# Kernel tuning notes

Measured on AMD Instinct MI355X. Metric: run time of the kernel, lower is better.

Reference implementation:

```python
import jax, jax.numpy as jnp
import numpy as np

N = 50000      # num nodes
E = 800000     # num edges (before self loops)
B = 50         # num graphs in batch
F_IN = 15
C = 64         # hidden_channels
H = 4          # num_heads
NEG_SLOPE = 0.2  # PyG GATConv default


def setup_inputs() -> dict:
    key = jax.random.key(0)
    ks = jax.random.split(key, 32)
    s = 0.05
    inp = {
        "x": jax.random.normal(ks[0], (N, F_IN), dtype=jnp.float32),
        "edge_index": jax.random.randint(ks[1], (2, E), 0, N, dtype=jnp.int32),
        "batch": jnp.sort(jax.random.randint(ks[2], (N,), 0, B, dtype=jnp.int32)),
        "W1": jax.random.normal(ks[3], (F_IN, H * C)) * s,
        "aS1": jax.random.normal(ks[4], (H, C)) * s,
        "aD1": jax.random.normal(ks[5], (H, C)) * s,
        "b1": jnp.zeros((H * C,)),
        "W2": jax.random.normal(ks[6], (H * C, H * C)) * s,
        "aS2": jax.random.normal(ks[7], (H, C)) * s,
        "aD2": jax.random.normal(ks[8], (H, C)) * s,
        "b2": jnp.zeros((H * C,)),
        # GAT layer 3: 256 -> 64, 1 head
        "W3": jax.random.normal(ks[9], (H * C, C)) * s,
        "aS3": jax.random.normal(ks[10], (1, C)) * s,
        "aD3": jax.random.normal(ks[11], (1, C)) * s,
        "b3": jnp.zeros((C,)),
        # node attention MLP: 64 -> 32 -> 1
        "Wna1": jax.random.normal(ks[12], (C, 32)) * s,
        "bna1": jnp.zeros((32,)),
        "Wna2": jax.random.normal(ks[13], (32, 1)) * s,
        "bna2": jnp.zeros((1,)),
        # graph classifier: 128 -> 128 -> 64 -> 1
        "Wc1": jax.random.normal(ks[14], (2 * C, 128)) * s,
        "bc1": jnp.zeros((128,)),
        "Wc2": jax.random.normal(ks[15], (128, 64)) * s,
        "bc2": jnp.zeros((64,)),
        "Wc3": jax.random.normal(ks[16], (64, 1)) * s,
        "bc3": jnp.zeros((1,)),
    }
    return inp


def _gat_conv(x, src, dst, W, a_src, a_dst, b, heads, ch):
    """PyG-style GATConv (add_self_loops=True, negative_slope=0.2, eval mode)."""
    n = x.shape[0]
    h = (x @ W).reshape(n, heads, ch)               # [N, H, C]
    alpha_s = jnp.einsum('nhc,hc->nh', h, a_src)    # per-node src score
    alpha_d = jnp.einsum('nhc,hc->nh', h, a_dst)
    loops = jnp.arange(n, dtype=src.dtype)
    s = jnp.concatenate([src, loops])               # [E+N]
    d = jnp.concatenate([dst, loops])
    e = jax.nn.leaky_relu(alpha_s[s] + alpha_d[d], NEG_SLOPE)   # [E+N, H]
    # segment softmax over incoming edges of each dst node
    m = jax.ops.segment_max(e, d, num_segments=n)
    ex = jnp.exp(e - m[d])
    denom = jax.ops.segment_sum(ex, d, num_segments=n)
    alpha = ex / denom[d]                           # [E+N, H]
    msg = h[s] * alpha[:, :, None]                  # [E+N, H, C]
    out = jax.ops.segment_sum(msg, d, num_segments=n)  # [N, H, C]
    return out.reshape(n, heads * ch) + b


def reference(x, edge_index, batch, W1, aS1, aD1, b1, W2, aS2, aD2, b2,
              W3, aS3, aD3, b3, Wna1, bna1, Wna2, bna2,
              Wc1, bc1, Wc2, bc2, Wc3, bc3):
    src, dst = edge_index[0], edge_index[1]
    x1 = jax.nn.elu(_gat_conv(x, src, dst, W1, aS1, aD1, b1, H, C))
    x2 = jax.nn.elu(_gat_conv(x1, src, dst, W2, aS2, aD2, b2, H, C))
    x3 = jax.nn.elu(_gat_conv(x2, src, dst, W3, aS3, aD3, b3, 1, C))  # [N, 64]

    # node attention: MLP then softmax over ALL nodes (dim=0, as in source)
    na = jax.nn.relu(x3 @ Wna1 + bna1) @ Wna2 + bna2   # [N, 1]
    node_attention = jax.nn.softmax(na, axis=0)

    # graph pooling
    ones = jnp.ones((x3.shape[0],), dtype=x3.dtype)
    cnt = jax.ops.segment_sum(ones, batch, num_segments=B)         # [B]
    mean = jax.ops.segment_sum(x3, batch, num_segments=B) / jnp.maximum(cnt, 1.0)[:, None]
    mx = jax.ops.segment_max(x3, batch, num_segments=B)
    mx = jnp.where(cnt[:, None] > 0, mx, 0.0)
    g = jnp.concatenate([mean, mx], axis=1)                        # [B, 128]

    h1 = jax.nn.relu(g @ Wc1 + bc1)
    h2 = jax.nn.relu(h1 @ Wc2 + bc2)
    risk = jax.nn.sigmoid(h2 @ Wc3 + bc3)                          # [B, 1]
    return (risk, node_attention)
```

## Files before the change

### kernel.cpp

```cpp
#include <hip/hip_runtime.h>
#include <math.h>

#define NN 50000
#define NP 50176
#define EE 800000
#define ETOT (EE + NN)
#define BB 50
#define PC 16
#define NGRP 12500

typedef unsigned short u16;
typedef unsigned char u8;
typedef __attribute__((ext_vector_type(8))) short short8;
typedef __attribute__((ext_vector_type(4))) float floatx4;
typedef __attribute__((ext_vector_type(2))) float floatx2;

__device__ __forceinline__ float b2f(u16 u) {
  return __int_as_float(((int)u) << 16);
}
__device__ __forceinline__ u16 f2b(float f) {
  unsigned u = __float_as_uint(f);
  unsigned r = (u + 0x7fffu + ((u >> 16) & 1u)) >> 16;
  return (u16)r;
}
__device__ __forceinline__ u8 f2f8(float v) {
  return (u8)(__builtin_amdgcn_cvt_pk_fp8_f32(v, v, 0, false) & 0xFF);
}
__device__ __forceinline__ float readlane_f(float v, int l) {
  return __int_as_float(__builtin_amdgcn_readlane(__float_as_int(v), l));
}

__global__ void count_kernel(const int* __restrict__ ei, int* __restrict__ cnt) {
  int e = blockIdx.x * blockDim.x + threadIdx.x;
  if (e >= ETOT) return;
  int d = (e < EE) ? ei[EE + e] : (e - EE);
  atomicAdd(&cnt[d], 1);
}

__global__ void scan1_kernel(const int* __restrict__ cnt, int* __restrict__ rowp,
                             int* __restrict__ part) {
  __shared__ int s[512];
  int t = threadIdx.x;
  int i = blockIdx.x * 512 + t;
  int v = (i < NN) ? cnt[i] : 0;
  s[t] = v;
  __syncthreads();
  for (int off = 1; off < 512; off <<= 1) {
    int add = (t >= off) ? s[t - off] : 0;
    __syncthreads();
    s[t] += add;
    __syncthreads();
  }
  if (i < NN) rowp[i] = s[t] - v;
  if (t == 511) part[blockIdx.x] = s[511];
}

__global__ void scan2_kernel(int* __restrict__ part, int* __restrict__ rowp) {
  __shared__ int s[128];
  int t = threadIdx.x;
  int v = (t < 98) ? part[t] : 0;
  s[t] = v;
  __syncthreads();
  for (int off = 1; off < 128; off <<= 1) {
    int add = (t >= off) ? s[t - off] : 0;
    __syncthreads();
    s[t] += add;
    __syncthreads();
  }
  if (t < 98) part[t] = s[t] - v;
  if (t == 97) rowp[NN] = s[97];
}

__global__ void scan3_kernel(int* __restrict__ rowp, const int* __restrict__ part) {
  int i = blockIdx.x * 512 + threadIdx.x;
  if (i < NN) rowp[i] += part[blockIdx.x];
}

__global__ void fill_kernel(const int* __restrict__ ei, const int* __restrict__ rowp,
                            int* __restrict__ cur, int* __restrict__ col) {
  int e = blockIdx.x * blockDim.x + threadIdx.x;
  if (e >= ETOT) return;
  int s, d;
  if (e < EE) { s = ei[e]; d = ei[EE + e]; } else { s = e - EE; d = s; }
  int p = atomicAdd(&cur[d], 1);
  col[rowp[d] + p] = s;
}

__global__ void prep_kernel(const float* __restrict__ x, const float* __restrict__ W1,
                            const float* __restrict__ W2, const float* __restrict__ W3,
                            u16* __restrict__ xb, u16* __restrict__ W1t,
                            u16* __restrict__ W2t, u16* __restrict__ W3t) {
  const int T0 = NP * 32, T1 = T0 + 8192, T2 = T1 + 65536, T3 = T2 + 16384;
  int i = blockIdx.x * 256 + threadIdx.x;
  if (i < T0) {
    int n = i >> 5, c = i & 31;
    xb[i] = (n < NN && c < 15) ? f2b(x[n * 15 + c]) : (u16)0;
  } else if (i < T1) {
    int j = i - T0, n = j >> 5, k = j & 31;
    W1t[j] = (k < 15) ? f2b(W1[k * 256 + n]) : (u16)0;
  } else if (i < T2) {
    int j = i - T1, n = j >> 8, k = j & 255;
    W2t[j] = f2b(W2[k * 256 + n]);
  } else if (i < T3) {
    int j = i - T2, n = j >> 8, k = j & 255;
    W3t[j] = f2b(W3[k * 64 + n]);
  }
}

template <int BK, bool F8>
__global__ __launch_bounds__(256) void gemm_bf16_kernel(
    const u16* __restrict__ A, const u16* __restrict__ Bt, u16* __restrict__ C,
    u8* __restrict__ C8, int K, int N, const float* __restrict__ aS,
    const float* __restrict__ aD, float* __restrict__ as_o,
    float* __restrict__ ad_o, int Hh) {
  __shared__ u16 Al[128][BK + 8];
  __shared__ u16 Bl[64][BK + 8];
  __shared__ float sS[4][64], sD[4][64];
  int R0 = blockIdx.x * 128, C0 = blockIdx.y * 64;
  int wid = threadIdx.x >> 6, lane = threadIdx.x & 63;
  int wr = (wid >> 1) * 64, wc = (wid & 1) * 32;
  int lrow = lane & 15, lk8 = (lane >> 4) * 8;
  int rq = (lane >> 4) * 4;
  const int Q4 = BK / 4;
  const int nA = 128 * Q4, nB = 64 * Q4;
  floatx4 acc[4][2];
#pragma unroll
  for (int i = 0; i < 4; ++i)
#pragma unroll
    for (int j = 0; j < 2; ++j) acc[i][j] = (floatx4){0.f, 0.f, 0.f, 0.f};

  for (int k0 = 0; k0 < K; k0 += BK) {
    for (int c = threadIdx.x; c < nA + nB; c += 256) {
      if (c < nA) {
        int r = c / Q4, o = (c % Q4) * 4;
        *(ushort4*)&Al[r][o] = *(const ushort4*)&A[(size_t)(R0 + r) * K + k0 + o];
      } else {
        int c2 = c - nA;
        int r = c2 / Q4, o = (c2 % Q4) * 4;
        *(ushort4*)&Bl[r][o] = *(const ushort4*)&Bt[(size_t)(C0 + r) * K + k0 + o];
      }
    }
    __syncthreads();
#pragma unroll
    for (int ks = 0; ks < BK / 32; ++ks) {
      short8 a[4], b[2];
#pragma unroll
      for (int i = 0; i < 4; ++i) a[i] = *(const short8*)&Al[wr + i * 16 + lrow][ks * 32 + lk8];
#pragma unroll
      for (int j = 0; j < 2; ++j) b[j] = *(const short8*)&Bl[wc + j * 16 + lrow][ks * 32 + lk8];
#pragma unroll
      for (int i = 0; i < 4; ++i)
#pragma unroll
        for (int j = 0; j < 2; ++j)
          acc[i][j] = __builtin_amdgcn_mfma_f32_16x16x32_bf16(a[i], b[j], acc[i][j], 0, 0, 0);
    }
    __syncthreads();
  }
#pragma unroll
  for (int i = 0; i < 4; ++i)
#pragma unroll
    for (int j = 0; j < 2; ++j)
#pragma unroll
      for (int q = 0; q < 4; ++q) {
        int gr = R0 + wr + i * 16 + rq + q;
        int gc = C0 + wc + j * 16 + lrow;
        if constexpr (F8)
          C8[(size_t)gr * N + gc] = f2f8(acc[i][j][q]);
        else
          C[(size_t)gr * N + gc] = f2b(acc[i][j][q]);
      }
  int hb = blockIdx.y * 64;
  float wS0 = aS[hb + wc + lrow], wS1 = aS[hb + wc + 16 + lrow];
  float wD0 = aD[hb + wc + lrow], wD1 = aD[hb + wc + 16 + lrow];
#pragma unroll
  for (int i = 0; i < 4; ++i)
#pragma unroll
    for (int q = 0; q < 4; ++q) {
      float vS = acc[i][0][q] * wS0 + acc[i][1][q] * wS1;
      float vD = acc[i][0][q] * wD0 + acc[i][1][q] * wD1;
#pragma unroll
      for (int o = 8; o; o >>= 1) {
        vS += __shfl_xor(vS, o, 64);
        vD += __shfl_xor(vD, o, 64);
      }
      if (lrow == 0) {
        int rl = i * 16 + rq + q;
        sS[wid][rl] = vS;
        sD[wid][rl] = vD;
      }
    }
  __syncthreads();
  if (threadIdx.x < 128) {
    int p = threadIdx.x >> 6, r = threadIdx.x & 63;
    int gr = R0 + p * 64 + r;
    as_o[(size_t)gr * Hh + blockIdx.y] = sS[2 * p][r] + sS[2 * p + 1][r];
    ad_o[(size_t)gr * Hh + blockIdx.y] = sD[2 * p][r] + sD[2 * p + 1][r];
  }
}

__global__ __launch_bounds__(256) void agg4_kernel(
    const u8* __restrict__ h8, const float* __restrict__ as_i,
    const float* __restrict__ ad_i, const int* __restrict__ rowp,
    const int* __restrict__ col, const float* __restrict__ bias,
    u16* __restrict__ xo) {
  __shared__ float exs[4][64][4];
  int wid = threadIdx.x >> 6, lane = threadIdx.x & 63;
  int hj = lane >> 4;
  int lq = lane << 2;
  for (int g = blockIdx.x; g < NGRP; g += gridDim.x) {
    int d = g * 4 + wid;
    int rp0 = rowp[d], deg = rowp[d + 1] - rp0;
    float4 add = *(const float4*)&ad_i[(size_t)d * 4];
    float a0 = 0.f, a1 = 0.f, a2 = 0.f, a3 = 0.f;
    float den0 = 0.f, den1 = 0.f, den2 = 0.f, den3 = 0.f;

    for (int base = 0; base < deg; base += 64) {
      int i = base + lane;
      bool valid = i < deg;
      int s = valid ? col[rp0 + i] : 0;
      float4 asv = *(const float4*)&as_i[(size_t)s * 4];
      float e0 = asv.x + add.x, e1 = asv.y + add.y, e2 = asv.z + add.z, e3 = asv.w + add.w;
      e0 = (e0 > 0.f) ? e0 : 0.2f * e0;
      e1 = (e1 > 0.f) ? e1 : 0.2f * e1;
      e2 = (e2 > 0.f) ? e2 : 0.2f * e2;
      e3 = (e3 > 0.f) ? e3 : 0.2f * e3;
      float x0 = valid ? __expf(e0) : 0.f;
      float x1 = valid ? __expf(e1) : 0.f;
      float x2 = valid ? __expf(e2) : 0.f;
      float x3 = valid ? __expf(e3) : 0.f;
      den0 += x0; den1 += x1; den2 += x2; den3 += x3;
      *(float4*)&exs[wid][lane][0] = make_float4(x0, x1, x2, x3);
      __threadfence_block();
      int cnt = min(64, deg - base);
      int k8 = cnt & ~7;
      for (int k = 0; k < k8; k += 8) {
        unsigned wv[8];
        float qv[8];
#pragma unroll
        for (int u = 0; u < 8; ++u) {
          int sk = __builtin_amdgcn_readlane(s, k + u);
          qv[u] = exs[wid][k + u][hj];
          wv[u] = *(const unsigned*)&h8[(size_t)sk * 256 + lq];
        }
#pragma unroll
        for (int u = 0; u < 8; ++u) {
          floatx2 lo = __builtin_amdgcn_cvt_pk_f32_fp8(wv[u], false);
          floatx2 hi = __builtin_amdgcn_cvt_pk_f32_fp8(wv[u], true);
          a0 += qv[u] * lo.x;
          a1 += qv[u] * lo.y;
          a2 += qv[u] * hi.x;
          a3 += qv[u] * hi.y;
        }
      }
      for (int k = k8; k < cnt; ++k) {
        int sk = __builtin_amdgcn_readlane(s, k);
        float qk = exs[wid][k][hj];
        unsigned wv = *(const unsigned*)&h8[(size_t)sk * 256 + lq];
        floatx2 lo = __builtin_amdgcn_cvt_pk_f32_fp8(wv, false);
        floatx2 hi = __builtin_amdgcn_cvt_pk_f32_fp8(wv, true);
        a0 += qk * lo.x;
        a1 += qk * lo.y;
        a2 += qk * hi.x;
        a3 += qk * hi.y;
      }
    }
#pragma unroll
    for (int o = 32; o; o >>= 1) {
      den0 += __shfl_xor(den0, o, 64);
      den1 += __shfl_xor(den1, o, 64);
      den2 += __shfl_xor(den2, o, 64);
      den3 += __shfl_xor(den3, o, 64);
    }
    float den = (hj == 0) ? den0 : (hj == 1) ? den1 : (hj == 2) ? den2 : den3;
    float inv = 1.f / den;
    float4 bv = *(const float4*)&bias[lq];
    float v0 = a0 * inv + bv.x;
    float v1 = a1 * inv + bv.y;
    float v2 = a2 * inv + bv.z;
    float v3 = a3 * inv + bv.w;
    v0 = (v0 > 0.f) ? v0 : expm1f(v0);
    v1 = (v1 > 0.f) ? v1 : expm1f(v1);
    v2 = (v2 > 0.f) ? v2 : expm1f(v2);
    v3 = (v3 > 0.f) ? v3 : expm1f(v3);
    ushort4 o4;
    o4.x = f2b(v0); o4.y = f2b(v1); o4.z = f2b(v2); o4.w = f2b(v3);
    ((ushort4*)xo)[(size_t)d * 64 + lane] = o4;
  }
}

__global__ __launch_bounds__(256) void agg1na_kernel(
    const u16* __restrict__ h, const float* __restrict__ as_i,
    const float* __restrict__ ad_i, const int* __restrict__ rowp,
    const int* __restrict__ col, const float* __restrict__ bias,
    float* __restrict__ xo, const float* __restrict__ Wna1,
    const float* __restrict__ bna1, const float* __restrict__ Wna2,
    const float* __restrict__ bna2, float* __restrict__ na) {
  __shared__ float Ws[2048];
  __shared__ float W2s[32];
  __shared__ float xrow[4][64];
  for (int i = threadIdx.x; i < 2048; i += 256) Ws[i] = Wna1[i];
  if (threadIdx.x < 32) W2s[threadIdx.x] = Wna2[threadIdx.x];
  __syncthreads();
  int wid = threadIdx.x >> 6, lane = threadIdx.x & 63;
  float b1v = bna1[lane & 31];
  float b2v = bna2[0];
  for (int g = blockIdx.x; g < NGRP; g += gridDim.x) {
    int d = g * 4 + wid;
    int rp0 = rowp[d], deg = rowp[d + 1] - rp0;
    float add = ad_i[d];
    float acc = 0.f, den = 0.f;
    for (int base = 0; base < deg; base += 64) {
      int i = base + lane;
      bool valid = i < deg;
      int s = valid ? col[rp0 + i] : 0;
      float e = as_i[s] + add;
      e = (e > 0.f) ? e : 0.2f * e;
      float ex = valid ? __expf(e) : 0.f;
      den += ex;
      int cnt = min(64, deg - base);
      int k8 = cnt & ~7;
      for (int k = 0; k < k8; k += 8) {
        int sA[8];
        float qA[8], hv[8];
#pragma unroll
        for (int u = 0; u < 8; ++u) {
          sA[u] = __builtin_amdgcn_readlane(s, k + u);
          qA[u] = readlane_f(ex, k + u);
        }
#pragma unroll
        for (int u = 0; u < 8; ++u) hv[u] = b2f(h[(size_t)sA[u] * 64 + lane]);
        float p0 = qA[0] * hv[0] + qA[1] * hv[1];
        float p1 = qA[2] * hv[2] + qA[3] * hv[3];
        float p2 = qA[4] * hv[4] + qA[5] * hv[5];
        float p3 = qA[6] * hv[6] + qA[7] * hv[7];
        acc += (p0 + p1) + (p2 + p3);
      }
      for (int k = k8; k < cnt; ++k) {
        int sk = __builtin_amdgcn_readlane(s, k);
        float qk = readlane_f(ex, k);
        acc += qk * b2f(h[(size_t)sk * 64 + lane]);
      }
    }
#pragma unroll
    for (int o = 32; o; o >>= 1) den += __shfl_xor(den, o, 64);
    float v = acc / den + bias[lane];
    v = (v > 0.f) ? v : expm1f(v);
    xo[(size_t)d * 64 + lane] = v;
    xrow[wid][lane] = v;
    __threadfence_block();
    int j = lane & 31;
    int coff = (lane >> 5) * 32;
    float hj = 0.f;
#pragma unroll
    for (int c = 0; c < 32; ++c) hj += xrow[wid][coff + c] * Ws[(coff + c) * 32 + j];
    hj += __shfl_xor(hj, 32, 64);
    hj += b1v;
    float r = fmaxf(hj, 0.f) * W2s[j];
#pragma unroll
    for (int o = 16; o; o >>= 1) r += __shfl_xor(r, o, 64);
    if (lane == 0) na[d] = __expf(r + b2v);
  }
}

__global__ void na_sum_kernel(const float* __restrict__ na, float* __restrict__ gsum) {
  __shared__ float s[4];
  float acc = 0.f;
  for (int i = blockIdx.x * blockDim.x + threadIdx.x; i < NN; i += gridDim.x * blockDim.x)
    acc += na[i];
  for (int o = 32; o; o >>= 1) acc += __shfl_xor(acc, o, 64);
  int wid = threadIdx.x >> 6, lane = threadIdx.x & 63;
  if (lane == 0) s[wid] = acc;
  __syncthreads();
  if (threadIdx.x == 0) atomicAdd(gsum, s[0] + s[1] + s[2] + s[3]);
}

__global__ void na_write_kernel(const float* __restrict__ na, const float* __restrict__ gsum,
                                float* __restrict__ out) {
  int n = blockIdx.x * blockDim.x + threadIdx.x;
  if (n >= NN) return;
  out[n] = na[n] / gsum[0];
}

__global__ void pool1_kernel(const float* __restrict__ x3, const int* __restrict__ batch,
                             float* __restrict__ ppsum, float* __restrict__ ppmax) {
  int b = blockIdx.x, c = blockIdx.y;
  int lane = threadIdx.x & 63, wid = threadIdx.x >> 6;
  int lo = 0, hi = NN;
  while (lo < hi) { int m = (lo + hi) >> 1; if (batch[m] < b) lo = m + 1; else hi = m; }
  int start = lo;
  lo = start; hi = NN;
  while (lo < hi) { int m = (lo + hi) >> 1; if (batch[m] < b + 1) lo = m + 1; else hi = m; }
  int end = lo;
  int len = end - start;
  int c0 = start + (int)((long)len * c / PC);
  int c1 = start + (int)((long)len * (c + 1) / PC);
  float acc = 0.f, mx = -INFINITY;
  for (int n = c0 + wid; n < c1; n += 4) {
    float v = x3[(size_t)n * 64 + lane];
    acc += v;
    mx = fmaxf(mx, v);
  }
  __shared__ float ssum[4][64], smax[4][64];
  ssum[wid][lane] = acc;
  smax[wid][lane] = mx;
  __syncthreads();
  if (wid == 0) {
    acc = ssum[0][lane] + ssum[1][lane] + ssum[2][lane] + ssum[3][lane];
    mx = fmaxf(fmaxf(smax[0][lane], smax[1][lane]), fmaxf(smax[2][lane], smax[3][lane]));
    size_t o = ((size_t)c * BB + b) * 64 + lane;
    ppsum[o] = acc;
    ppmax[o] = mx;
  }
}

__global__ void pool2cls_kernel(const float* __restrict__ ppsum, const float* __restrict__ ppmax,
                                const int* __restrict__ batch, const float* __restrict__ Wc1,
                                const float* __restrict__ bc1, const float* __restrict__ Wc2,
                                const float* __restrict__ bc2, const float* __restrict__ Wc3,
                                const float* __restrict__ bc3, float* __restrict__ out) {
  __shared__ float g[128], h1[128], h2[64], scnt;
  int b = blockIdx.x, t = threadIdx.x;
  if (t == 0) {
    int lo = 0, hi = NN;
    while (lo < hi) { int m = (lo + hi) >> 1; if (batch[m] < b) lo = m + 1; else hi = m; }
    int start = lo;
    lo = start; hi = NN;
    while (lo < hi) { int m = (lo + hi) >> 1; if (batch[m] < b + 1) lo = m + 1; else hi = m; }
    scnt = (float)(lo - start);
  }
  float s = 0.f, m = -INFINITY;
  if (t < 64) {
#pragma unroll
    for (int c = 0; c < PC; ++c) {
      size_t o = ((size_t)c * BB + b) * 64 + t;
      s += ppsum[o];
      m = fmaxf(m, ppmax[o]);
    }
  }
  __syncthreads();
  float cnt = scnt;
  if (t < 64) {
    g[t] = (cnt > 0.f) ? s / fmaxf(cnt, 1.f) : 0.f;
    g[64 + t] = (cnt > 0.f) ? m : 0.f;
  }
  __syncthreads();
  float v = bc1[t];
  for (int k = 0; k < 128; ++k) v += g[k] * Wc1[k * 128 + t];
  h1[t] = fmaxf(v, 0.f);
  __syncthreads();
  if (t < 64) {
    float v2 = bc2[t];
    for (int k = 0; k < 128; ++k) v2 += h1[k] * Wc2[k * 64 + t];
    h2[t] = fmaxf(v2, 0.f);
  }
  __syncthreads();
  if (t == 0) {
    float z = bc3[0];
    for (int k = 0; k < 64; ++k) z += h2[k] * Wc3[k];
    out[b] = 1.f / (1.f + expf(-z));
  }
}

extern "C" void kernel_launch(void* const* d_in, const int* in_sizes, int n_in,
                              void* d_out, int out_size, void* d_ws, size_t ws_size,
                              hipStream_t stream) {
  const float* x    = (const float*)d_in[0];
  const int*   ei   = (const int*)d_in[1];
  const int*   batch= (const int*)d_in[2];
  const float* W1 = (const float*)d_in[3];
  const float* aS1= (const float*)d_in[4];
  const float* aD1= (const float*)d_in[5];
  const float* b1 = (const float*)d_in[6];
  const float* W2 = (const float*)d_in[7];
  const float* aS2= (const float*)d_in[8];
  const float* aD2= (const float*)d_in[9];
  const float* b2 = (const float*)d_in[10];
  const float* W3 = (const float*)d_in[11];
  const float* aS3= (const float*)d_in[12];
  const float* aD3= (const float*)d_in[13];
  const float* b3 = (const float*)d_in[14];
  const float* Wna1=(const float*)d_in[15];
  const float* bna1=(const float*)d_in[16];
  const float* Wna2=(const float*)d_in[17];
  const float* bna2=(const float*)d_in[18];
  const float* Wc1=(const float*)d_in[19];
  const float* bc1=(const float*)d_in[20];
  const float* Wc2=(const float*)d_in[21];
  const float* bc2=(const float*)d_in[22];
  const float* Wc3=(const float*)d_in[23];
  const float* bc3=(const float*)d_in[24];
  float* out = (float*)d_out;

  char* w = (char*)d_ws;
  size_t off = 0;
  auto alloc = [&](size_t bytes) {
    void* p = w + off;
    off = (off + bytes + 255) & ~(size_t)255;
    return p;
  };
  u16* xb   = (u16*)alloc((size_t)NP * 32 * 2);
  u16* bufA = (u16*)alloc((size_t)NP * 256 * 2);
  u16* bufB = (u16*)alloc((size_t)NP * 256 * 2);
  u8*  h8   = (u8*)alloc((size_t)NP * 256);
  u16* W1t  = (u16*)alloc((size_t)256 * 32 * 2);
  u16* W2t  = (u16*)alloc((size_t)256 * 256 * 2);
  u16* W3t  = (u16*)alloc((size_t)64 * 256 * 2);
  float* asb  = (float*)alloc((size_t)NP * 4 * 4);
  float* adb  = (float*)alloc((size_t)NP * 4 * 4);
  float* nab  = (float*)alloc((size_t)NN * 4);
  int* rowp = (int*)alloc((size_t)(NN + 1) * 4);
  int* cntb = (int*)alloc((size_t)NN * 4);
  int* curb = (int*)alloc((size_t)NN * 4);
  float* gsum = (float*)alloc(256);
  size_t zspan = (size_t)((char*)gsum + 256 - (char*)cntb);
  int* colb = (int*)alloc((size_t)ETOT * 4);
  int* part = (int*)alloc(128 * 4);
  float* ppsum = (float*)alloc((size_t)PC * BB * 64 * 4);
  float* ppmax = (float*)alloc((size_t)PC * BB * 64 * 4);
  float* x3 = (float*)bufB;
  (void)ws_size; (void)in_sizes; (void)n_in; (void)out_size;

  hipMemsetAsync(cntb, 0, zspan, stream);

  count_kernel<<<(ETOT + 255) / 256, 256, 0, stream>>>(ei, cntb);
  scan1_kernel<<<98, 512, 0, stream>>>(cntb, rowp, part);
  scan2_kernel<<<1, 128, 0, stream>>>(part, rowp);
  scan3_kernel<<<98, 512, 0, stream>>>(rowp, part);
  fill_kernel<<<(ETOT + 255) / 256, 256, 0, stream>>>(ei, rowp, curb, colb);

  const int PREP_TOT = NP * 32 + 8192 + 65536 + 16384;
  prep_kernel<<<(PREP_TOT + 255) / 256, 256, 0, stream>>>(x, W1, W2, W3, xb, W1t, W2t, W3t);

  const int GX = NP / 128;
  const int PG = 2048;
  gemm_bf16_kernel<32, true><<<dim3(GX, 4), 256, 0, stream>>>(
      xb, W1t, nullptr, h8, 32, 256, aS1, aD1, asb, adb, 4);
  agg4_kernel<<<PG, 256, 0, stream>>>(h8, asb, adb, rowp, colb, b1, bufB);
  gemm_bf16_kernel<64, true><<<dim3(GX, 4), 256, 0, stream>>>(
      bufB, W2t, nullptr, h8, 256, 256, aS2, aD2, asb, adb, 4);
  agg4_kernel<<<PG, 256, 0, stream>>>(h8, asb, adb, rowp, colb, b2, bufB);
  gemm_bf16_kernel<64, false><<<dim3(GX, 1), 256, 0, stream>>>(
      bufB, W3t, bufA, nullptr, 256, 64, aS3, aD3, asb, adb, 1);
  agg1na_kernel<<<PG, 256, 0, stream>>>(bufA, asb, adb, rowp, colb, b3, x3,
                                        Wna1, bna1, Wna2, bna2, nab);

  na_sum_kernel<<<196, 256, 0, stream>>>(nab, gsum);
  na_write_kernel<<<(NN + 255) / 256, 256, 0, stream>>>(nab, gsum, out + BB);
  pool1_kernel<<<dim3(BB, PC), 256, 0, stream>>>(x3, batch, ppsum, ppmax);
  pool2cls_kernel<<<BB, 128, 0, stream>>>(ppsum, ppmax, batch, Wc1, bc1, Wc2, bc2,
                                          Wc3, bc3, out);
}
```

Baseline: 389.0 us.

## Precompute edge attention exponentials in separate per-edge kernels before aggregation

```diff
diff --git a/kernel.cpp b/kernel.cpp
--- a/kernel.cpp
+++ b/kernel.cpp
@@ -7,7 +7,6 @@
 #define ETOT (EE + NN)
 #define BB 50
 #define PC 16
-#define NGRP 12500
 
 typedef unsigned short u16;
 typedef unsigned char u8;
@@ -77,13 +76,16 @@
 }
 
 __global__ void fill_kernel(const int* __restrict__ ei, const int* __restrict__ rowp,
-                            int* __restrict__ cur, int* __restrict__ col) {
+                            int* __restrict__ cur, int* __restrict__ col,
+                            int* __restrict__ dstb) {
   int e = blockIdx.x * blockDim.x + threadIdx.x;
   if (e >= ETOT) return;
   int s, d;
   if (e < EE) { s = ei[e]; d = ei[EE + e]; } else { s = e - EE; d = s; }
   int p = atomicAdd(&cur[d], 1);
-  col[rowp[d] + p] = s;
+  int idx = rowp[d] + p;
+  col[idx] = s;
+  dstb[idx] = d;
 }
 
 __global__ void prep_kernel(const float* __restrict__ x, const float* __restrict__ W1,
@@ -198,103 +200,118 @@
   }
 }
 
+template <int LAYER>
+__global__ void escore4_kernel(const float* __restrict__ as_i, const float* __restrict__ ad_i,
+                               const int* __restrict__ col, const int* __restrict__ dstb,
+                               float4* __restrict__ exl) {
+  int i = blockIdx.x * 256 + threadIdx.x;
+  if (i >= ETOT) return;
+  int s = col[i], d = dstb[i];
+  float4 a = *(const float4*)&as_i[(size_t)s * 4];
+  float4 b = *(const float4*)&ad_i[(size_t)d * 4];
+  float e0 = a.x + b.x, e1 = a.y + b.y, e2 = a.z + b.z, e3 = a.w + b.w;
+  e0 = (e0 > 0.f) ? e0 : 0.2f * e0;
+  e1 = (e1 > 0.f) ? e1 : 0.2f * e1;
+  e2 = (e2 > 0.f) ? e2 : 0.2f * e2;
+  e3 = (e3 > 0.f) ? e3 : 0.2f * e3;
+  exl[i] = make_float4(__expf(e0), __expf(e1), __expf(e2), __expf(e3));
+}
+
+__global__ void escore1_kernel(const float* __restrict__ as_i, const float* __restrict__ ad_i,
+                               const int* __restrict__ col, const int* __restrict__ dstb,
+                               float* __restrict__ exl) {
+  int i = blockIdx.x * 256 + threadIdx.x;
+  if (i >= ETOT) return;
+  float e = as_i[col[i]] + ad_i[dstb[i]];
+  e = (e > 0.f) ? e : 0.2f * e;
+  exl[i] = __expf(e);
+}
+
+template <int LAYER>
 __global__ __launch_bounds__(256) void agg4_kernel(
-    const u8* __restrict__ h8, const float* __restrict__ as_i,
-    const float* __restrict__ ad_i, const int* __restrict__ rowp,
-    const int* __restrict__ col, const float* __restrict__ bias,
-    u16* __restrict__ xo) {
+    const u8* __restrict__ h8, const float4* __restrict__ exl,
+    const int* __restrict__ rowp, const int* __restrict__ col,
+    const float* __restrict__ bias, u16* __restrict__ xo) {
   __shared__ float exs[4][64][4];
   int wid = threadIdx.x >> 6, lane = threadIdx.x & 63;
+  int d = blockIdx.x * 4 + wid;
+  int rp0 = rowp[d], deg = rowp[d + 1] - rp0;
   int hj = lane >> 4;
   int lq = lane << 2;
-  for (int g = blockIdx.x; g < NGRP; g += gridDim.x) {
-    int d = g * 4 + wid;
-    int rp0 = rowp[d], deg = rowp[d + 1] - rp0;
-    float4 add = *(const float4*)&ad_i[(size_t)d * 4];
-    float a0 = 0.f, a1 = 0.f, a2 = 0.f, a3 = 0.f;
-    float den0 = 0.f, den1 = 0.f, den2 = 0.f, den3 = 0.f;
-
-    for (int base = 0; base < deg; base += 64) {
-      int i = base + lane;
-      bool valid = i < deg;
-      int s = valid ? col[rp0 + i] : 0;
-      float4 asv = *(const float4*)&as_i[(size_t)s * 4];
-      float e0 = asv.x + add.x, e1 = asv.y + add.y, e2 = asv.z + add.z, e3 = asv.w + add.w;
-      e0 = (e0 > 0.f) ? e0 : 0.2f * e0;
-      e1 = (e1 > 0.f) ? e1 : 0.2f * e1;
-      e2 = (e2 > 0.f) ? e2 : 0.2f * e2;
-      e3 = (e3 > 0.f) ? e3 : 0.2f * e3;
-      float x0 = valid ? __expf(e0) : 0.f;
-      float x1 = valid ? __expf(e1) : 0.f;
-      float x2 = valid ? __expf(e2) : 0.f;
-      float x3 = valid ? __expf(e3) : 0.f;
-      den0 += x0; den1 += x1; den2 += x2; den3 += x3;
-      *(float4*)&exs[wid][lane][0] = make_float4(x0, x1, x2, x3);
-      __threadfence_block();
-      int cnt = min(64, deg - base);
-      int k8 = cnt & ~7;
-      for (int k = 0; k < k8; k += 8) {
-        unsigned wv[8];
-        float qv[8];
-#pragma unroll
-        for (int u = 0; u < 8; ++u) {
-          int sk = __builtin_amdgcn_readlane(s, k + u);
-          qv[u] = exs[wid][k + u][hj];
-          wv[u] = *(const unsigned*)&h8[(size_t)sk * 256 + lq];
-        }
-#pragma unroll
-        for (int u = 0; u < 8; ++u) {
-          floatx2 lo = __builtin_amdgcn_cvt_pk_f32_fp8(wv[u], false);
-          floatx2 hi = __builtin_amdgcn_cvt_pk_f32_fp8(wv[u], true);
-          a0 += qv[u] * lo.x;
-          a1 += qv[u] * lo.y;
-          a2 += qv[u] * hi.x;
-          a3 += qv[u] * hi.y;
-        }
-      }
-      for (int k = k8; k < cnt; ++k) {
-        int sk = __builtin_amdgcn_readlane(s, k);
-        float qk = exs[wid][k][hj];
-        unsigned wv = *(const unsigned*)&h8[(size_t)sk * 256 + lq];
-        floatx2 lo = __builtin_amdgcn_cvt_pk_f32_fp8(wv, false);
-        floatx2 hi = __builtin_amdgcn_cvt_pk_f32_fp8(wv, true);
-        a0 += qk * lo.x;
-        a1 += qk * lo.y;
-        a2 += qk * hi.x;
-        a3 += qk * hi.y;
-      }
-    }
-#pragma unroll
-    for (int o = 32; o; o >>= 1) {
-      den0 += __shfl_xor(den0, o, 64);
-      den1 += __shfl_xor(den1, o, 64);
-      den2 += __shfl_xor(den2, o, 64);
-      den3 += __shfl_xor(den3, o, 64);
-    }
-    float den = (hj == 0) ? den0 : (hj == 1) ? den1 : (hj == 2) ? den2 : den3;
-    float inv = 1.f / den;
-    float4 bv = *(const float4*)&bias[lq];
-    float v0 = a0 * inv + bv.x;
-    float v1 = a1 * inv + bv.y;
-    float v2 = a2 * inv + bv.z;
-    float v3 = a3 * inv + bv.w;
-    v0 = (v0 > 0.f) ? v0 : expm1f(v0);
-    v1 = (v1 > 0.f) ? v1 : expm1f(v1);
-    v2 = (v2 > 0.f) ? v2 : expm1f(v2);
-    v3 = (v3 > 0.f) ? v3 : expm1f(v3);
-    ushort4 o4;
-    o4.x = f2b(v0); o4.y = f2b(v1); o4.z = f2b(v2); o4.w = f2b(v3);
-    ((ushort4*)xo)[(size_t)d * 64 + lane] = o4;
-  }
+  float a0 = 0.f, a1 = 0.f, a2 = 0.f, a3 = 0.f;
+  float den0 = 0.f, den1 = 0.f, den2 = 0.f, den3 = 0.f;
+
+  for (int base = 0; base < deg; base += 64) {
+    int i = base + lane;
+    bool valid = i < deg;
+    int s = valid ? col[rp0 + i] : 0;
+    float4 xv = valid ? exl[rp0 + i] : make_float4(0.f, 0.f, 0.f, 0.f);
+    den0 += xv.x; den1 += xv.y; den2 += xv.z; den3 += xv.w;
+    *(float4*)&exs[wid][lane][0] = xv;
+    __threadfence_block();
+    int cnt = min(64, deg - base);
+    int k8 = cnt & ~7;
+    for (int k = 0; k < k8; k += 8) {
+      unsigned wv[8];
+      float qv[8];
+#pragma unroll
+      for (int u = 0; u < 8; ++u) {
+        int sk = __builtin_amdgcn_readlane(s, k + u);
+        qv[u] = exs[wid][k + u][hj];
+        wv[u] = *(const unsigned*)&h8[(size_t)sk * 256 + lq];
+      }
+#pragma unroll
+      for (int u = 0; u < 8; ++u) {
+        floatx2 lo = __builtin_amdgcn_cvt_pk_f32_fp8(wv[u], false);
+        floatx2 hi = __builtin_amdgcn_cvt_pk_f32_fp8(wv[u], true);
+        a0 += qv[u] * lo.x;
+        a1 += qv[u] * lo.y;
+        a2 += qv[u] * hi.x;
+        a3 += qv[u] * hi.y;
+      }
+    }
+    for (int k = k8; k < cnt; ++k) {
+      int sk = __builtin_amdgcn_readlane(s, k);
+      float qk = exs[wid][k][hj];
+      unsigned wv = *(const unsigned*)&h8[(size_t)sk * 256 + lq];
+      floatx2 lo = __builtin_amdgcn_cvt_pk_f32_fp8(wv, false);
+      floatx2 hi = __builtin_amdgcn_cvt_pk_f32_fp8(wv, true);
+      a0 += qk * lo.x;
+      a1 += qk * lo.y;
+      a2 += qk * hi.x;
+      a3 += qk * hi.y;
+    }
+  }
+#pragma unroll
+  for (int o = 32; o; o >>= 1) {
+    den0 += __shfl_xor(den0, o, 64);
+    den1 += __shfl_xor(den1, o, 64);
+    den2 += __shfl_xor(den2, o, 64);
+    den3 += __shfl_xor(den3, o, 64);
+  }
+  float den = (hj == 0) ? den0 : (hj == 1) ? den1 : (hj == 2) ? den2 : den3;
+  float inv = 1.f / den;
+  float4 bv = *(const float4*)&bias[lq];
+  float v0 = a0 * inv + bv.x;
+  float v1 = a1 * inv + bv.y;
+  float v2 = a2 * inv + bv.z;
+  float v3 = a3 * inv + bv.w;
+  v0 = (v0 > 0.f) ? v0 : expm1f(v0);
+  v1 = (v1 > 0.f) ? v1 : expm1f(v1);
+  v2 = (v2 > 0.f) ? v2 : expm1f(v2);
+  v3 = (v3 > 0.f) ? v3 : expm1f(v3);
+  ushort4 o4;
+  o4.x = f2b(v0); o4.y = f2b(v1); o4.z = f2b(v2); o4.w = f2b(v3);
+  ((ushort4*)xo)[(size_t)d * 64 + lane] = o4;
 }
 
 __global__ __launch_bounds__(256) void agg1na_kernel(
-    const u16* __restrict__ h, const float* __restrict__ as_i,
-    const float* __restrict__ ad_i, const int* __restrict__ rowp,
-    const int* __restrict__ col, const float* __restrict__ bias,
-    float* __restrict__ xo, const float* __restrict__ Wna1,
-    const float* __restrict__ bna1, const float* __restrict__ Wna2,
-    const float* __restrict__ bna2, float* __restrict__ na) {
+    const u16* __restrict__ h, const float* __restrict__ exl,
+    const int* __restrict__ rowp, const int* __restrict__ col,
+    const float* __restrict__ bias, float* __restrict__ xo,
+    const float* __restrict__ Wna1, const float* __restrict__ bna1,
+    const float* __restrict__ Wna2, const float* __restrict__ bna2,
+    float* __restrict__ na) {
   __shared__ float Ws[2048];
   __shared__ float W2s[32];
   __shared__ float xrow[4][64];
@@ -302,64 +319,57 @@
   if (threadIdx.x < 32) W2s[threadIdx.x] = Wna2[threadIdx.x];
   __syncthreads();
   int wid = threadIdx.x >> 6, lane = threadIdx.x & 63;
-  float b1v = bna1[lane & 31];
-  float b2v = bna2[0];
-  for (int g = blockIdx.x; g < NGRP; g += gridDim.x) {
-    int d = g * 4 + wid;
-    int rp0 = rowp[d], deg = rowp[d + 1] - rp0;
-    float add = ad_i[d];
-    float acc = 0.f, den = 0.f;
-    for (int base = 0; base < deg; base += 64) {
-      int i = base + lane;
-      bool valid = i < deg;
-      int s = valid ? col[rp0 + i] : 0;
-      float e = as_i[s] + add;
-      e = (e > 0.f) ? e : 0.2f * e;
-      float ex = valid ? __expf(e) : 0.f;
-      den += ex;
-      int cnt = min(64, deg - base);
-      int k8 = cnt & ~7;
-      for (int k = 0; k < k8; k += 8) {
-        int sA[8];
-        float qA[8], hv[8];
-#pragma unroll
-        for (int u = 0; u < 8; ++u) {
-          sA[u] = __builtin_amdgcn_readlane(s, k + u);
-          qA[u] = readlane_f(ex, k + u);
-        }
-#pragma unroll
-        for (int u = 0; u < 8; ++u) hv[u] = b2f(h[(size_t)sA[u] * 64 + lane]);
-        float p0 = qA[0] * hv[0] + qA[1] * hv[1];
-        float p1 = qA[2] * hv[2] + qA[3] * hv[3];
-        float p2 = qA[4] * hv[4] + qA[5] * hv[5];
-        float p3 = qA[6] * hv[6] + qA[7] * hv[7];
-        acc += (p0 + p1) + (p2 + p3);
-      }
-      for (int k = k8; k < cnt; ++k) {
-        int sk = __builtin_amdgcn_readlane(s, k);
-        float qk = readlane_f(ex, k);
-        acc += qk * b2f(h[(size_t)sk * 64 + lane]);
-      }
-    }
-#pragma unroll
-    for (int o = 32; o; o >>= 1) den += __shfl_xor(den, o, 64);
-    float v = acc / den + bias[lane];
-    v = (v > 0.f) ? v : expm1f(v);
-    xo[(size_t)d * 64 + lane] = v;
-    xrow[wid][lane] = v;
-    __threadfence_block();
-    int j = lane & 31;
-    int coff = (lane >> 5) * 32;
-    float hj = 0.f;
-#pragma unroll
-    for (int c = 0; c < 32; ++c) hj += xrow[wid][coff + c] * Ws[(coff + c) * 32 + j];
-    hj += __shfl_xor(hj, 32, 64);
-    hj += b1v;
-    float r = fmaxf(hj, 0.f) * W2s[j];
-#pragma unroll
-    for (int o = 16; o; o >>= 1) r += __shfl_xor(r, o, 64);
-    if (lane == 0) na[d] = __expf(r + b2v);
-  }
+  int d = blockIdx.x * 4 + wid;
+  int rp0 = rowp[d], deg = rowp[d + 1] - rp0;
+  float acc = 0.f, den = 0.f;
+  for (int base = 0; base < deg; base += 64) {
+    int i = base + lane;
+    bool valid = i < deg;
+    int s = valid ? col[rp0 + i] : 0;
+    float ex = valid ? exl[rp0 + i] : 0.f;
+    den += ex;
+    int cnt = min(64, deg - base);
+    int k8 = cnt & ~7;
+    for (int k = 0; k < k8; k += 8) {
+      int sA[8];
+      float qA[8], hv[8];
+#pragma unroll
+      for (int u = 0; u < 8; ++u) {
+        sA[u] = __builtin_amdgcn_readlane(s, k + u);
+        qA[u] = readlane_f(ex, k + u);
+      }
+#pragma unroll
+      for (int u = 0; u < 8; ++u) hv[u] = b2f(h[(size_t)sA[u] * 64 + lane]);
+      float p0 = qA[0] * hv[0] + qA[1] * hv[1];
+      float p1 = qA[2] * hv[2] + qA[3] * hv[3];
+      float p2 = qA[4] * hv[4] + qA[5] * hv[5];
+      float p3 = qA[6] * hv[6] + qA[7] * hv[7];
+      acc += (p0 + p1) + (p2 + p3);
+    }
+    for (int k = k8; k < cnt; ++k) {
+      int sk = __builtin_amdgcn_readlane(s, k);
+      float qk = readlane_f(ex, k);
+      acc += qk * b2f(h[(size_t)sk * 64 + lane]);
+    }
+  }
+#pragma unroll
+  for (int o = 32; o; o >>= 1) den += __shfl_xor(den, o, 64);
+  float v = acc / den + bias[lane];
+  v = (v > 0.f) ? v : expm1f(v);
+  xo[(size_t)d * 64 + lane] = v;
+  xrow[wid][lane] = v;
+  __threadfence_block();
+  int j = lane & 31;
+  int coff = (lane >> 5) * 32;
+  float hj = 0.f;
+#pragma unroll
+  for (int c = 0; c < 32; ++c) hj += xrow[wid][coff + c] * Ws[(coff + c) * 32 + j];
+  hj += __shfl_xor(hj, 32, 64);
+  hj += bna1[j];
+  float r = fmaxf(hj, 0.f) * W2s[j];
+#pragma unroll
+  for (int o = 16; o; o >>= 1) r += __shfl_xor(r, o, 64);
+  if (lane == 0) na[d] = __expf(r + bna2[0]);
 }
 
 __global__ void na_sum_kernel(const float* __restrict__ na, float* __restrict__ gsum) {
@@ -508,6 +518,8 @@
   float* asb  = (float*)alloc((size_t)NP * 4 * 4);
   float* adb  = (float*)alloc((size_t)NP * 4 * 4);
   float* nab  = (float*)alloc((size_t)NN * 4);
+  float4* exl4 = (float4*)alloc((size_t)ETOT * 16);
+  int* dstb = (int*)alloc((size_t)ETOT * 4);
   int* rowp = (int*)alloc((size_t)(NN + 1) * 4);
   int* cntb = (int*)alloc((size_t)NN * 4);
   int* curb = (int*)alloc((size_t)NN * 4);
@@ -518,6 +530,7 @@
   float* ppsum = (float*)alloc((size_t)PC * BB * 64 * 4);
   float* ppmax = (float*)alloc((size_t)PC * BB * 64 * 4);
   float* x3 = (float*)bufB;
+  float* exl1 = (float*)exl4;
   (void)ws_size; (void)in_sizes; (void)n_in; (void)out_size;
 
   hipMemsetAsync(cntb, 0, zspan, stream);
@@ -526,23 +539,26 @@
   scan1_kernel<<<98, 512, 0, stream>>>(cntb, rowp, part);
   scan2_kernel<<<1, 128, 0, stream>>>(part, rowp);
   scan3_kernel<<<98, 512, 0, stream>>>(rowp, part);
-  fill_kernel<<<(ETOT + 255) / 256, 256, 0, stream>>>(ei, rowp, curb, colb);
+  fill_kernel<<<(ETOT + 255) / 256, 256, 0, stream>>>(ei, rowp, curb, colb, dstb);
 
   const int PREP_TOT = NP * 32 + 8192 + 65536 + 16384;
   prep_kernel<<<(PREP_TOT + 255) / 256, 256, 0, stream>>>(x, W1, W2, W3, xb, W1t, W2t, W3t);
 
   const int GX = NP / 128;
-  const int PG = 2048;
+  const int EG = (ETOT + 255) / 256;
   gemm_bf16_kernel<32, true><<<dim3(GX, 4), 256, 0, stream>>>(
       xb, W1t, nullptr, h8, 32, 256, aS1, aD1, asb, adb, 4);
-  agg4_kernel<<<PG, 256, 0, stream>>>(h8, asb, adb, rowp, colb, b1, bufB);
+  escore4_kernel<1><<<EG, 256, 0, stream>>>(asb, adb, colb, dstb, exl4);
+  agg4_kernel<1><<<12500, 256, 0, stream>>>(h8, exl4, rowp, colb, b1, bufB);
   gemm_bf16_kernel<64, true><<<dim3(GX, 4), 256, 0, stream>>>(
       bufB, W2t, nullptr, h8, 256, 256, aS2, aD2, asb, adb, 4);
-  agg4_kernel<<<PG, 256, 0, stream>>>(h8, asb, adb, rowp, colb, b2, bufB);
+  escore4_kernel<2><<<EG, 256, 0, stream>>>(asb, adb, colb, dstb, exl4);
+  agg4_kernel<2><<<12500, 256, 0, stream>>>(h8, exl4, rowp, colb, b2, bufB);
   gemm_bf16_kernel<64, false><<<dim3(GX, 1), 256, 0, stream>>>(
       bufB, W3t, bufA, nullptr, 256, 64, aS3, aD3, asb, adb, 1);
-  agg1na_kernel<<<PG, 256, 0, stream>>>(bufA, asb, adb, rowp, colb, b3, x3,
-                                        Wna1, bna1, Wna2, bna2, nab);
+  escore1_kernel<<<EG, 256, 0, stream>>>(asb, adb, colb, dstb, exl1);
+  agg1na_kernel<<<12500, 256, 0, stream>>>(bufA, exl1, rowp, colb, b3, x3,
+                                           Wna1, bna1, Wna2, bna2, nab);
 
   na_sum_kernel<<<196, 256, 0, stream>>>(nab, gsum);
   na_write_kernel<<<(NN + 255) / 256, 256, 0, stream>>>(nab, gsum, out + BB);
```

After: 377.1 us. -3.1%, faster.
